# Performance work log

Measured on AMD Instinct MI355X. Metric: run time of the kernel, lower is better.

## Reference

```python
import jax, jax.numpy as jnp
import numpy as np

# Instant-NGP hash-encoding constants
PI = np.array([1, 2654435761, 805459861], dtype=np.uint32)
NUM_LEVELS = 16
MIN_RES = 16
MAX_RES = 512
T = 524288  # max entries per level (2**19)
D_EMBED = 2
N_POINTS = 2097152

# 8 binary corner offsets of a unit cube, shape [8, 3]
CORNERS = np.array([[(c >> d) & 1 for d in range(3)] for c in range(8)], dtype=np.int32)


def level_params():
    """Static per-level resolution, table size, offset, hashed flag."""
    b = (MAX_RES / MIN_RES) ** (1.0 / (NUM_LEVELS - 1))
    res = [int(np.floor(MIN_RES * b ** i)) for i in range(NUM_LEVELS)]
    sizes = [min((r + 1) ** 3, T) for r in res]
    offsets = np.concatenate([[0], np.cumsum(sizes)[:-1]]).astype(np.int32)
    hashed = [(r + 1) ** 3 > T for r in res]
    return res, sizes, offsets, hashed


RES, SIZES, OFFSETS, HASHED = level_params()
TOTAL_ENTRIES = int(np.sum(SIZES))


def setup_inputs() -> dict:
    key = jax.random.key(0)
    k1, k2 = jax.random.split(key)
    coords = jax.random.uniform(k1, (N_POINTS, 3), dtype=jnp.float32)
    embeddings = jax.random.normal(k2, (TOTAL_ENTRIES, D_EMBED), dtype=jnp.float32)
    return {"coords": coords, "embeddings": embeddings}


def _encode(coords, embeddings):
    corners = jnp.asarray(CORNERS)            # [8, 3] int32
    corner_mask = jnp.asarray(CORNERS, bool)  # [8, 3]
    pi = jnp.asarray(PI)                      # [3] uint32
    outs = []
    for lvl in range(NUM_LEVELS):
        res = RES[lvl]
        scaled = coords * res                                   # [N, 3]
        base = jnp.floor(scaled)
        frac = scaled - base                                    # [N, 3]
        # integer corner coords, clipped to valid grid range [0, res]
        c = jnp.clip(base.astype(jnp.int32)[:, None, :] + corners[None], 0, res)  # [N, 8, 3]
        if HASHED[lvl]:
            h = c.astype(jnp.uint32) * pi                        # wraparound mul, [N, 8, 3]
            idx = (h[..., 0] ^ h[..., 1] ^ h[..., 2]) % jnp.uint32(SIZES[lvl])
            idx = idx.astype(jnp.int32)                          # [N, 8]
        else:
            s = res + 1
            idx = c[..., 0] + c[..., 1] * s + c[..., 2] * (s * s)  # [N, 8]
        emb = embeddings[OFFSETS[lvl] + idx]                     # gather: [N, 8, d_embed]
        # trilinear weights: prod over dims of frac (corner=1) or 1-frac (corner=0)
        w = jnp.prod(jnp.where(corner_mask[None], frac[:, None, :], 1.0 - frac[:, None, :]), axis=-1)  # [N, 8]
        outs.append(jnp.einsum("nc,ncd->nd", w, emb))            # [N, d_embed]
    return jnp.concatenate(outs, axis=-1)                        # [N, L*d_embed]


def reference(coords, embeddings):
    return _encode(coords, embeddings)
```

## Files before the change

kernel.cpp:

```cpp
#include <hip/hip_runtime.h>
#include <math.h>

namespace {
constexpr int NPTS = 1 << 21;
constexpr int NLVL = 16;
constexpr unsigned TMASK = 0x7FFFFu;
constexpr unsigned PI1 = 2654435761u;
constexpr unsigned PI2 = 805459861u;
constexpr int BLK = 512;
constexpr int PTS_PER_BLK = 512;
constexpr int NBLK = NPTS / PTS_PER_BLK;
constexpr int NGRID = 7;
constexpr int NHASH = 9;
constexpr int BRES = 64;
constexpr int NBKT = BRES * BRES * BRES;

typedef float f2 __attribute__((ext_vector_type(2)));
typedef float f4 __attribute__((ext_vector_type(4)));
typedef unsigned u4 __attribute__((ext_vector_type(4)));

struct Params {
  float resf[NLVL];
  int off[NLVL];
  int cellOffB[NGRID];
  int hOffB[NHASH];
};

__device__ __forceinline__ int swz(int pt) { return (pt ^ (pt >> 3)) & 7; }

__device__ __forceinline__ unsigned bfrne(float x) {
  unsigned f = __float_as_uint(x);
  return (f + 0x7FFFu + ((f >> 16) & 1u)) >> 16;
}
__device__ __forceinline__ unsigned packbf(f2 e) {
  return bfrne(e.x) | (bfrne(e.y) << 16);
}
__device__ __forceinline__ float bflo(unsigned u) {
  return __uint_as_float(u << 16);
}
__device__ __forceinline__ float bfhi(unsigned u) {
  return __uint_as_float(u & 0xFFFF0000u);
}
__device__ __forceinline__ unsigned sel4(f4 v, int k) {
  float g = (k & 2) ? ((k & 1) ? v.w : v.z) : ((k & 1) ? v.y : v.x);
  return __float_as_uint(g);
}
__device__ __forceinline__ int bucket_of(float cx, float cy, float cz) {
  return (int)(cx * 64.f) + ((int)(cy * 64.f) << 6) + ((int)(cz * 64.f) << 12);
}
}

__global__ __launch_bounds__(256) void repack_all(const f2* __restrict__ emb,
                                                  char* __restrict__ ws,
                                                  Params p) {
  int y = (int)blockIdx.y;
  int t = (int)blockIdx.x * 256 + (int)threadIdx.x;
  if (y >= NGRID) {
    int h = y - NGRID;
    int off = p.off[7], hob = p.hOffB[0];
    if (h == 1) { off = p.off[8]; hob = p.hOffB[1]; }
    if (h == 2) { off = p.off[9]; hob = p.hOffB[2]; }
    if (h == 3) { off = p.off[10]; hob = p.hOffB[3]; }
    if (h == 4) { off = p.off[11]; hob = p.hOffB[4]; }
    if (h == 5) { off = p.off[12]; hob = p.hOffB[5]; }
    if (h == 6) { off = p.off[13]; hob = p.hOffB[6]; }
    if (h == 7) { off = p.off[14]; hob = p.hOffB[7]; }
    if (h == 8) { off = p.off[15]; hob = p.hOffB[8]; }
    ((unsigned*)(ws + (size_t)hob))[t] = packbf(emb[off + t]);
    return;
  }
  float rf = p.resf[0];
  int off = p.off[0], cob = p.cellOffB[0];
  if (y == 1) { rf = p.resf[1]; off = p.off[1]; cob = p.cellOffB[1]; }
  if (y == 2) { rf = p.resf[2]; off = p.off[2]; cob = p.cellOffB[2]; }
  if (y == 3) { rf = p.resf[3]; off = p.off[3]; cob = p.cellOffB[3]; }
  if (y == 4) { rf = p.resf[4]; off = p.off[4]; cob = p.cellOffB[4]; }
  if (y == 5) { rf = p.resf[5]; off = p.off[5]; cob = p.cellOffB[5]; }
  if (y == 6) { rf = p.resf[6]; off = p.off[6]; cob = p.cellOffB[6]; }
  int res = (int)rf;
  if (t >= res * res * res) return;
  int x = t % res, q = t / res, yy = q % res, z = q / res;
  int s = res + 1, s2 = s * s;
  const f2* base = emb + off + (x + yy * s + z * s2);
  u4 d0, d1;
  d0.x = packbf(base[0]);       d0.y = packbf(base[1]);
  d0.z = packbf(base[s]);       d0.w = packbf(base[s + 1]);
  d1.x = packbf(base[s2]);      d1.y = packbf(base[s2 + 1]);
  d1.z = packbf(base[s2 + s]);  d1.w = packbf(base[s2 + s + 1]);
  u4* dst = (u4*)(ws + (size_t)cob + (size_t)t * 32);
  dst[0] = d0; dst[1] = d1;
}

__global__ __launch_bounds__(256) void repack_grid(const f2* __restrict__ emb,
                                                   char* __restrict__ ws,
                                                   Params p) {
  int lvl = (int)blockIdx.y;
  float rf = p.resf[0];
  int off = p.off[0], cob = p.cellOffB[0];
  if (lvl == 1) { rf = p.resf[1]; off = p.off[1]; cob = p.cellOffB[1]; }
  if (lvl == 2) { rf = p.resf[2]; off = p.off[2]; cob = p.cellOffB[2]; }
  if (lvl == 3) { rf = p.resf[3]; off = p.off[3]; cob = p.cellOffB[3]; }
  if (lvl == 4) { rf = p.resf[4]; off = p.off[4]; cob = p.cellOffB[4]; }
  if (lvl == 5) { rf = p.resf[5]; off = p.off[5]; cob = p.cellOffB[5]; }
  if (lvl == 6) { rf = p.resf[6]; off = p.off[6]; cob = p.cellOffB[6]; }
  int res = (int)rf;
  int t = (int)blockIdx.x * 256 + (int)threadIdx.x;
  if (t >= res * res * res) return;
  int x = t % res, q = t / res, y = q % res, z = q / res;
  int s = res + 1, s2 = s * s;
  const f2* base = emb + off + (x + y * s + z * s2);
  u4 d0, d1;
  d0.x = packbf(base[0]);       d0.y = packbf(base[1]);
  d0.z = packbf(base[s]);       d0.w = packbf(base[s + 1]);
  d1.x = packbf(base[s2]);      d1.y = packbf(base[s2 + 1]);
  d1.z = packbf(base[s2 + s]);  d1.w = packbf(base[s2 + s + 1]);
  u4* dst = (u4*)(ws + (size_t)cob + (size_t)t * 32);
  dst[0] = d0; dst[1] = d1;
}

__global__ __launch_bounds__(256) void hist_k(const float* __restrict__ coords,
                                              unsigned* __restrict__ cnt) {
  int t = (int)blockIdx.x * 256 + (int)threadIdx.x;
  const f4* C = (const f4*)(coords + (size_t)t * 12);
  f4 a = C[0], b = C[1], c = C[2];
  atomicAdd(&cnt[bucket_of(a.x, a.y, a.z)], 1u);
  atomicAdd(&cnt[bucket_of(a.w, b.x, b.y)], 1u);
  atomicAdd(&cnt[bucket_of(b.z, b.w, c.x)], 1u);
  atomicAdd(&cnt[bucket_of(c.y, c.z, c.w)], 1u);
}

__global__ __launch_bounds__(256) void scan1_k(const unsigned* __restrict__ cnt,
                                               unsigned* __restrict__ scanA,
                                               unsigned* __restrict__ bsum) {
  __shared__ unsigned s[256];
  int t = (int)threadIdx.x, i = (int)blockIdx.x * 256 + t;
  unsigned v = cnt[i];
  s[t] = v;
  __syncthreads();
  for (int d = 1; d < 256; d <<= 1) {
    unsigned x = (t >= d) ? s[t - d] : 0u;
    __syncthreads();
    s[t] += x;
    __syncthreads();
  }
  scanA[i] = s[t] - v;
  if (t == 255) bsum[blockIdx.x] = s[255];
}

__global__ __launch_bounds__(1024) void scan2_k(unsigned* __restrict__ bsum) {
  __shared__ unsigned s[1024];
  int t = (int)threadIdx.x;
  unsigned v = bsum[t];
  s[t] = v;
  __syncthreads();
  for (int d = 1; d < 1024; d <<= 1) {
    unsigned x = (t >= d) ? s[t - d] : 0u;
    __syncthreads();
    s[t] += x;
    __syncthreads();
  }
  bsum[t] = s[t] - v;
}

__global__ __launch_bounds__(256) void scat_k(const float* __restrict__ coords,
                                              unsigned* __restrict__ scanA,
                                              const unsigned* __restrict__ bsum,
                                              f4* __restrict__ sorted) {
  int t = (int)blockIdx.x * 256 + (int)threadIdx.x;
  const f4* C = (const f4*)(coords + (size_t)t * 12);
  f4 a = C[0], b = C[1], c = C[2];
  unsigned n0 = (unsigned)(t * 4);
  int b0 = bucket_of(a.x, a.y, a.z);
  unsigned s0 = atomicAdd(&scanA[b0], 1u) + bsum[b0 >> 8];
  f4 v0; v0.x = a.x; v0.y = a.y; v0.z = a.z; v0.w = __uint_as_float(n0);
  sorted[s0] = v0;
  int b1 = bucket_of(a.w, b.x, b.y);
  unsigned s1 = atomicAdd(&scanA[b1], 1u) + bsum[b1 >> 8];
  f4 v1; v1.x = a.w; v1.y = b.x; v1.z = b.y; v1.w = __uint_as_float(n0 + 1u);
  sorted[s1] = v1;
  int b2 = bucket_of(b.z, b.w, c.x);
  unsigned s2 = atomicAdd(&scanA[b2], 1u) + bsum[b2 >> 8];
  f4 v2; v2.x = b.z; v2.y = b.w; v2.z = c.x; v2.w = __uint_as_float(n0 + 2u);
  sorted[s2] = v2;
  int b3 = bucket_of(c.y, c.z, c.w);
  unsigned s3 = atomicAdd(&scanA[b3], 1u) + bsum[b3 >> 8];
  f4 v3; v3.x = c.y; v3.y = c.z; v3.z = c.w; v3.w = __uint_as_float(n0 + 3u);
  sorted[s3] = v3;
}

struct GB {
  f4 l0, l1;
  float wx0, wx1, w00, w10, w01, w11;
};

template <int LVL>
__device__ __forceinline__ void gridb_issue(const Params& p,
                                            const char* __restrict__ ws,
                                            float cx, float cy, float cz,
                                            GB& s) {
  float rf = p.resf[LVL];
  int res = (int)rf;
  float sx = cx * rf, sy = cy * rf, sz = cz * rf;
  float bx = floorf(sx), by = floorf(sy), bz = floorf(sz);
  float fx = sx - bx, fy = sy - by, fz = sz - bz;
  int ix = (int)bx, iy = (int)by, iz = (int)bz;
  int cell = (iz * res + iy) * res + ix;
  const f4* src = (const f4*)(ws + (size_t)p.cellOffB[LVL] + (size_t)cell * 32);
  s.l0 = src[0]; s.l1 = src[1];
  float wy0 = 1.f - fy, wy1 = fy, wz0 = 1.f - fz, wz1 = fz;
  s.wx0 = 1.f - fx; s.wx1 = fx;
  s.w00 = wy0 * wz0; s.w10 = wy1 * wz0; s.w01 = wy0 * wz1; s.w11 = wy1 * wz1;
}

__device__ __forceinline__ f2 gridb_consume(const GB& s) {
  float a0 = 0.f, a1 = 0.f;
  unsigned u;
  u = __float_as_uint(s.l0.x); a0 = fmaf(s.wx0 * s.w00, bflo(u), a0); a1 = fmaf(s.wx0 * s.w00, bfhi(u), a1);
  u = __float_as_uint(s.l0.y); a0 = fmaf(s.wx1 * s.w00, bflo(u), a0); a1 = fmaf(s.wx1 * s.w00, bfhi(u), a1);
  u = __float_as_uint(s.l0.z); a0 = fmaf(s.wx0 * s.w10, bflo(u), a0); a1 = fmaf(s.wx0 * s.w10, bfhi(u), a1);
  u = __float_as_uint(s.l0.w); a0 = fmaf(s.wx1 * s.w10, bflo(u), a0); a1 = fmaf(s.wx1 * s.w10, bfhi(u), a1);
  u = __float_as_uint(s.l1.x); a0 = fmaf(s.wx0 * s.w01, bflo(u), a0); a1 = fmaf(s.wx0 * s.w01, bfhi(u), a1);
  u = __float_as_uint(s.l1.y); a0 = fmaf(s.wx1 * s.w01, bflo(u), a0); a1 = fmaf(s.wx1 * s.w01, bfhi(u), a1);
  u = __float_as_uint(s.l1.z); a0 = fmaf(s.wx0 * s.w11, bflo(u), a0); a1 = fmaf(s.wx0 * s.w11, bfhi(u), a1);
  u = __float_as_uint(s.l1.w); a0 = fmaf(s.wx1 * s.w11, bflo(u), a0); a1 = fmaf(s.wx1 * s.w11, bfhi(u), a1);
  f2 r; r.x = a0; r.y = a1;
  return r;
}

template <int LVL>
__device__ __forceinline__ f2 grid_direct(const Params& p,
                                          const f2* __restrict__ emb, float cx,
                                          float cy, float cz) {
  float rf = p.resf[LVL];
  int res = (int)rf;
  int s = res + 1, s2 = s * s;
  const f2* tab = emb + p.off[LVL];
  float sx = cx * rf, sy = cy * rf, sz = cz * rf;
  float bx = floorf(sx), by = floorf(sy), bz = floorf(sz);
  float fx = sx - bx, fy = sy - by, fz = sz - bz;
  int ix = (int)bx, iy = (int)by, iz = (int)bz;
  int bse = ix + iy * s + iz * s2;
  f2 e0 = tab[bse], e1 = tab[bse + 1];
  f2 e2 = tab[bse + s], e3 = tab[bse + s + 1];
  f2 e4 = tab[bse + s2], e5 = tab[bse + s2 + 1];
  f2 e6 = tab[bse + s2 + s], e7 = tab[bse + s2 + s + 1];
  float wx0 = 1.f - fx, wx1 = fx, wy0 = 1.f - fy, wy1 = fy;
  float wz0 = 1.f - fz, wz1 = fz;
  float w00 = wy0 * wz0, w10 = wy1 * wz0, w01 = wy0 * wz1, w11 = wy1 * wz1;
  float a0 = 0.f, a1 = 0.f;
  a0 = fmaf(wx0 * w00, e0.x, a0); a1 = fmaf(wx0 * w00, e0.y, a1);
  a0 = fmaf(wx1 * w00, e1.x, a0); a1 = fmaf(wx1 * w00, e1.y, a1);
  a0 = fmaf(wx0 * w10, e2.x, a0); a1 = fmaf(wx0 * w10, e2.y, a1);
  a0 = fmaf(wx1 * w10, e3.x, a0); a1 = fmaf(wx1 * w10, e3.y, a1);
  a0 = fmaf(wx0 * w01, e4.x, a0); a1 = fmaf(wx0 * w01, e4.y, a1);
  a0 = fmaf(wx1 * w01, e5.x, a0); a1 = fmaf(wx1 * w01, e5.y, a1);
  a0 = fmaf(wx0 * w11, e6.x, a0); a1 = fmaf(wx0 * w11, e6.y, a1);
  a0 = fmaf(wx1 * w11, e7.x, a0); a1 = fmaf(wx1 * w11, e7.y, a1);
  f2 r; r.x = a0; r.y = a1;
  return r;
}

struct HB {
  f4 cA0, cA1, cA2, cA3;
  unsigned uB0, uB1, uB2, uB3;
  float wA0, wB0, wA1, wB1, wA2, wB2, wA3, wB3;
  int kA0, kA1, kA2, kA3, kB0, kB1, kB2, kB3;
  bool sameChunk;
};

template <int LVL>
__device__ __forceinline__ void hashb_issue(const Params& p,
                                            const char* __restrict__ ws,
                                            float cx, float cy, float cz,
                                            HB& s) {
  float rf = p.resf[LVL];
  const f4* tab = (const f4*)(ws + (size_t)p.hOffB[LVL - 7]);
  const unsigned* t32 = (const unsigned*)tab;
  float sx = cx * rf, sy = cy * rf, sz = cz * rf;
  float bx = floorf(sx), by = floorf(sy), bz = floorf(sz);
  float fx = sx - bx, fy = sy - by, fz = sz - bz;
  unsigned ix = (unsigned)(int)bx, iy = (unsigned)(int)by,
           iz = (unsigned)(int)bz;
  unsigned jx = ix + 1u;
  unsigned ty0 = iy * PI1, ty1 = ty0 + PI1;
  unsigned tz0 = iz * PI2, tz1 = tz0 + PI2;
  unsigned e00 = ty0 ^ tz0, e10 = ty1 ^ tz0, e01 = ty0 ^ tz1, e11 = ty1 ^ tz1;
  float wx0 = 1.f - fx, wx1 = fx, wy0 = 1.f - fy, wy1 = fy;
  float wz0 = 1.f - fz, wz1 = fz;
  float w00 = wy0 * wz0, w10 = wy1 * wz0, w01 = wy0 * wz1, w11 = wy1 * wz1;
  unsigned iA0 = (ix ^ e00) & TMASK, iB0 = (jx ^ e00) & TMASK;
  unsigned iA1 = (ix ^ e10) & TMASK, iB1 = (jx ^ e10) & TMASK;
  unsigned iA2 = (ix ^ e01) & TMASK, iB2 = (jx ^ e01) & TMASK;
  unsigned iA3 = (ix ^ e11) & TMASK, iB3 = (jx ^ e11) & TMASK;
  s.sameChunk = (ix & 3u) != 3u;
  s.uB0 = 0u; s.uB1 = 0u; s.uB2 = 0u; s.uB3 = 0u;
  if (!s.sameChunk) {
    s.uB0 = t32[iB0]; s.uB1 = t32[iB1];
    s.uB2 = t32[iB2]; s.uB3 = t32[iB3];
  }
  s.cA0 = tab[iA0 >> 2]; s.cA1 = tab[iA1 >> 2];
  s.cA2 = tab[iA2 >> 2]; s.cA3 = tab[iA3 >> 2];
  s.kA0 = (int)(iA0 & 3u); s.kA1 = (int)(iA1 & 3u);
  s.kA2 = (int)(iA2 & 3u); s.kA3 = (int)(iA3 & 3u);
  s.kB0 = (int)(iB0 & 3u); s.kB1 = (int)(iB1 & 3u);
  s.kB2 = (int)(iB2 & 3u); s.kB3 = (int)(iB3 & 3u);
  s.wA0 = wx0 * w00; s.wB0 = wx1 * w00;
  s.wA1 = wx0 * w10; s.wB1 = wx1 * w10;
  s.wA2 = wx0 * w01; s.wB2 = wx1 * w01;
  s.wA3 = wx0 * w11; s.wB3 = wx1 * w11;
}

__device__ __forceinline__ void hbpair(f4 cA, unsigned uBl, int kA, int kB,
                                       bool same, float wA, float wB,
                                       float& a0, float& a1) {
  unsigned uA = sel4(cA, kA);
  unsigned uB = same ? sel4(cA, kB) : uBl;
  a0 = fmaf(wA, bflo(uA), a0); a1 = fmaf(wA, bfhi(uA), a1);
  a0 = fmaf(wB, bflo(uB), a0); a1 = fmaf(wB, bfhi(uB), a1);
}

__device__ __forceinline__ f2 hashb_consume(const HB& s) {
  float a0 = 0.f, a1 = 0.f;
  hbpair(s.cA0, s.uB0, s.kA0, s.kB0, s.sameChunk, s.wA0, s.wB0, a0, a1);
  hbpair(s.cA1, s.uB1, s.kA1, s.kB1, s.sameChunk, s.wA1, s.wB1, a0, a1);
  hbpair(s.cA2, s.uB2, s.kA2, s.kB2, s.sameChunk, s.wA2, s.wB2, a0, a1);
  hbpair(s.cA3, s.uB3, s.kA3, s.kB3, s.sameChunk, s.wA3, s.wB3, a0, a1);
  f2 r; r.x = a0; r.y = a1;
  return r;
}

struct HS {
  f4 lo0, hi0, lo1, hi1, lo2, hi2, lo3, hi3;
  float wA0, wB0, wA1, wB1, wA2, wB2, wA3, wB3;
  int oA0, oB0, oA1, oB1, oA2, oB2, oA3, oB3;
};

template <int LVL>
__device__ __forceinline__ void hash_issue(const Params& p,
                                           const f2* __restrict__ emb,
                                           float cx, float cy, float cz,
                                           HS& s) {
  float rf = p.resf[LVL];
  const f2* tab = emb + p.off[LVL];
  float sx = cx * rf, sy = cy * rf, sz = cz * rf;
  float bx = floorf(sx), by = floorf(sy), bz = floorf(sz);
  float fx = sx - bx, fy = sy - by, fz = sz - bz;
  unsigned ix = (unsigned)(int)bx, iy = (unsigned)(int)by,
           iz = (unsigned)(int)bz;
  unsigned jx = ix + 1u;
  unsigned ty0 = iy * PI1, ty1 = ty0 + PI1;
  unsigned tz0 = iz * PI2, tz1 = tz0 + PI2;
  unsigned e00 = ty0 ^ tz0, e10 = ty1 ^ tz0, e01 = ty0 ^ tz1, e11 = ty1 ^ tz1;
  float wx0 = 1.f - fx, wx1 = fx, wy0 = 1.f - fy, wy1 = fy;
  float wz0 = 1.f - fz, wz1 = fz;
  float w00 = wy0 * wz0, w10 = wy1 * wz0, w01 = wy0 * wz1, w11 = wy1 * wz1;
  unsigned iA, iB;
  iA = (ix ^ e00) & TMASK; iB = (jx ^ e00) & TMASK;
  s.oA0 = (int)(iA & 1u); s.oB0 = (int)(iB & 1u);
  s.lo0 = *(const f4*)(tab + (iA & ~1u)); s.hi0 = *(const f4*)(tab + (iB & ~1u));
  s.wA0 = wx0 * w00; s.wB0 = wx1 * w00;
  iA = (ix ^ e10) & TMASK; iB = (jx ^ e10) & TMASK;
  s.oA1 = (int)(iA & 1u); s.oB1 = (int)(iB & 1u);
  s.lo1 = *(const f4*)(tab + (iA & ~1u)); s.hi1 = *(const f4*)(tab + (iB & ~1u));
  s.wA1 = wx0 * w10; s.wB1 = wx1 * w10;
  iA = (ix ^ e01) & TMASK; iB = (jx ^ e01) & TMASK;
  s.oA2 = (int)(iA & 1u); s.oB2 = (int)(iB & 1u);
  s.lo2 = *(const f4*)(tab + (iA & ~1u)); s.hi2 = *(const f4*)(tab + (iB & ~1u));
  s.wA2 = wx0 * w01; s.wB2 = wx1 * w01;
  iA = (ix ^ e11) & TMASK; iB = (jx ^ e11) & TMASK;
  s.oA3 = (int)(iA & 1u); s.oB3 = (int)(iB & 1u);
  s.lo3 = *(const f4*)(tab + (iA & ~1u)); s.hi3 = *(const f4*)(tab + (iB & ~1u));
  s.wA3 = wx0 * w11; s.wB3 = wx1 * w11;
}

__device__ __forceinline__ void hpair2(f4 lo, f4 hi, int oA, int oB, float wA,
                                       float wB, float& a0, float& a1) {
  float eAx = oA ? lo.z : lo.x, eAy = oA ? lo.w : lo.y;
  float eBx = oB ? hi.z : hi.x, eBy = oB ? hi.w : hi.y;
  a0 = fmaf(wA, eAx, a0); a1 = fmaf(wA, eAy, a1);
  a0 = fmaf(wB, eBx, a0); a1 = fmaf(wB, eBy, a1);
}

__device__ __forceinline__ f2 hash_consume(const HS& s) {
  float a0 = 0.f, a1 = 0.f;
  hpair2(s.lo0, s.hi0, s.oA0, s.oB0, s.wA0, s.wB0, a0, a1);
  hpair2(s.lo1, s.hi1, s.oA1, s.oB1, s.wA1, s.wB1, a0, a1);
  hpair2(s.lo2, s.hi2, s.oA2, s.oB2, s.wA2, s.wB2, a0, a1);
  hpair2(s.lo3, s.hi3, s.oA3, s.oB3, s.wA3, s.wB3, a0, a1);
  f2 r; r.x = a0; r.y = a1;
  return r;
}

template <int LVL, int MODE>
__device__ __forceinline__ void do_phase(const Params& p,
                                         const f2* __restrict__ emb,
                                         const char* __restrict__ ws, float cx,
                                         float cy, float cz, int pt,
                                         unsigned* lds) {
  f2 r;
  if constexpr (LVL < NGRID) {
    if constexpr (MODE < 2) {
      GB s;
      gridb_issue<LVL>(p, ws, cx, cy, cz, s);
      r = gridb_consume(s);
    } else {
      r = grid_direct<LVL>(p, emb, cx, cy, cz);
    }
  } else {
    if constexpr (MODE == 0) {
      HB s;
      hashb_issue<LVL>(p, ws, cx, cy, cz, s);
      r = hashb_consume(s);
    } else {
      HS s;
      hash_issue<LVL>(p, emb, cx, cy, cz, s);
      r = hash_consume(s);
    }
  }
  lds[pt * 8 + ((LVL & 7) ^ swz(pt))] = packbf(r);
}

template <bool SORTED>
__device__ __forceinline__ void readout(float* __restrict__ out,
                                        const unsigned* lds,
                                        const unsigned* oiLds, int n0, int h,
                                        int tid) {
#pragma unroll
  for (int j = 0; j < 4; ++j) {
    int f = tid + BLK * j;
    int pt = f >> 2, k = f & 3;
    int s = swz(pt);
    unsigned u0 = lds[pt * 8 + ((2 * k) ^ s)];
    unsigned u1 = lds[pt * 8 + ((2 * k + 1) ^ s)];
    f4 o4; o4.x = bflo(u0); o4.y = bfhi(u0); o4.z = bflo(u1); o4.w = bfhi(u1);
    size_t base = SORTED ? (size_t)oiLds[pt] * 32 : (size_t)(n0 + pt) * 32;
    __builtin_nontemporal_store(o4, (f4*)(out + base + h * 16 + k * 4));
  }
}

template <int MODE, bool SORTED>
__global__ __launch_bounds__(BLK, 4) void henc(const float* __restrict__ coords,
                                               const f2* __restrict__ emb,
                                               float* __restrict__ out,
                                               const char* __restrict__ ws,
                                               const f4* __restrict__ sorted,
                                               Params p) {
  __shared__ unsigned lds[PTS_PER_BLK * 8];
  __shared__ unsigned oiLds[PTS_PER_BLK];
  const int tid = (int)threadIdx.x;
  const int n0 = (int)blockIdx.x * PTS_PER_BLK;
  const int pt = tid;

  float cx, cy, cz;
  if constexpr (SORTED) {
    f4 s0 = sorted[n0 + pt];
    cx = s0.x; cy = s0.y; cz = s0.z;
    oiLds[pt] = __float_as_uint(s0.w);
  } else {
    cx = coords[3 * (n0 + pt) + 0];
    cy = coords[3 * (n0 + pt) + 1];
    cz = coords[3 * (n0 + pt) + 2];
  }

  do_phase<0, MODE>(p, emb, ws, cx, cy, cz, pt, lds);
  do_phase<1, MODE>(p, emb, ws, cx, cy, cz, pt, lds);
  do_phase<2, MODE>(p, emb, ws, cx, cy, cz, pt, lds);
  do_phase<3, MODE>(p, emb, ws, cx, cy, cz, pt, lds);
  do_phase<4, MODE>(p, emb, ws, cx, cy, cz, pt, lds);
  do_phase<5, MODE>(p, emb, ws, cx, cy, cz, pt, lds);
  do_phase<6, MODE>(p, emb, ws, cx, cy, cz, pt, lds);
  do_phase<7, MODE>(p, emb, ws, cx, cy, cz, pt, lds);
  __syncthreads();
  readout<SORTED>(out, lds, oiLds, n0, 0, tid);
  __syncthreads();

  do_phase<8, MODE>(p, emb, ws, cx, cy, cz, pt, lds);
  do_phase<9, MODE>(p, emb, ws, cx, cy, cz, pt, lds);
  do_phase<10, MODE>(p, emb, ws, cx, cy, cz, pt, lds);
  do_phase<11, MODE>(p, emb, ws, cx, cy, cz, pt, lds);
  do_phase<12, MODE>(p, emb, ws, cx, cy, cz, pt, lds);
  do_phase<13, MODE>(p, emb, ws, cx, cy, cz, pt, lds);
  do_phase<14, MODE>(p, emb, ws, cx, cy, cz, pt, lds);
  do_phase<15, MODE>(p, emb, ws, cx, cy, cz, pt, lds);
  __syncthreads();
  readout<SORTED>(out, lds, oiLds, n0, 1, tid);
}

extern "C" void kernel_launch(void* const* d_in, const int* in_sizes, int n_in,
                              void* d_out, int out_size, void* d_ws,
                              size_t ws_size, hipStream_t stream) {
  const float* coords = (const float*)d_in[0];
  const f2* emb = (const f2*)d_in[1];
  float* out = (float*)d_out;
  char* ws = (char*)d_ws;

  Params p;
  double b = pow(32.0, 1.0 / 15.0);
  long long cum = 0, cellCum = 0;
  int resMax = 64;
  for (int i = 0; i < NLVL; ++i) {
    int r = (int)floor(16.0 * pow(b, (double)i));
    p.resf[i] = (float)r;
    p.off[i] = (int)cum;
    long long e3 = (long long)(r + 1) * (r + 1) * (r + 1);
    cum += e3 > 524288 ? 524288 : e3;
    if (i < NGRID) {
      p.cellOffB[i] = (int)(cellCum * 32);
      cellCum += (long long)r * r * r;
      if (i == NGRID - 1) resMax = r;
    }
  }
  long long gridB = ((cellCum * 32 + 63) / 64) * 64;
  for (int h = 0; h < NHASH; ++h)
    p.hOffB[h] = (int)(gridB + (long long)h * (524288 * 4));
  size_t needB = (size_t)gridB;
  size_t needA = (size_t)(gridB + 9LL * 524288 * 4);

  size_t cntOff = (needA + 255) & ~(size_t)255;
  size_t scanOff = cntOff + (size_t)NBKT * 4;
  size_t bsumOff = scanOff + (size_t)NBKT * 4;
  size_t sortedOff = (bsumOff + 4096 + 255) & ~(size_t)255;
  size_t needS = sortedOff + (size_t)NPTS * 16;

  int mode = ws_size >= needA ? 0 : (ws_size >= needB ? 1 : 2);
  bool doSort = ws_size >= needS;

  if (mode == 0) {
    repack_all<<<dim3(524288 / 256, NLVL), dim3(256), 0, stream>>>(emb, ws, p);
    if (doSort) {
      unsigned* cnt = (unsigned*)(ws + cntOff);
      unsigned* scanA = (unsigned*)(ws + scanOff);
      unsigned* bsum = (unsigned*)(ws + bsumOff);
      f4* sorted = (f4*)(ws + sortedOff);
      hipMemsetAsync(cnt, 0, (size_t)NBKT * 4, stream);
      hist_k<<<dim3(NPTS / 4 / 256), dim3(256), 0, stream>>>(coords, cnt);
      scan1_k<<<dim3(NBKT / 256), dim3(256), 0, stream>>>(cnt, scanA, bsum);
      scan2_k<<<dim3(1), dim3(1024), 0, stream>>>(bsum);
      scat_k<<<dim3(NPTS / 4 / 256), dim3(256), 0, stream>>>(coords, scanA,
                                                             bsum, sorted);
      henc<0, true><<<dim3(NBLK), dim3(BLK), 0, stream>>>(coords, emb, out, ws,
                                                          sorted, p);
    } else {
      henc<0, false><<<dim3(NBLK), dim3(BLK), 0, stream>>>(coords, emb, out,
                                                           ws, nullptr, p);
    }
  } else if (mode == 1) {
    int bx = (resMax * resMax * resMax + 255) / 256;
    repack_grid<<<dim3(bx, NGRID), dim3(256), 0, stream>>>(emb, ws, p);
    henc<1, false><<<dim3(NBLK), dim3(BLK), 0, stream>>>(coords, emb, out, ws,
                                                         nullptr, p);
  } else {
    henc<2, false><<<dim3(NBLK), dim3(BLK), 0, stream>>>(coords, emb, out, ws,
                                                         nullptr, p);
  }
}
```

Measured before the change: 467.7 us.

## Fuse point bucket sort into a single cooperative kernel with grid syncs

```diff
diff --git a/kernel.cpp b/kernel.cpp
--- a/kernel.cpp
+++ b/kernel.cpp
@@ -1,5 +1,8 @@
 #include <hip/hip_runtime.h>
+#include <hip/hip_cooperative_groups.h>
 #include <math.h>
+
+namespace cg = cooperative_groups;
 
 namespace {
 constexpr int NPTS = 1 << 21;
@@ -14,6 +17,8 @@
 constexpr int NHASH = 9;
 constexpr int BRES = 64;
 constexpr int NBKT = BRES * BRES * BRES;
+constexpr int SORT_BLKS = 2048;
+constexpr int SORT_THR = 256;
 
 typedef float f2 __attribute__((ext_vector_type(2)));
 typedef float f4 __attribute__((ext_vector_type(4)));
@@ -116,6 +121,81 @@
   d1.z = packbf(base[s2 + s]);  d1.w = packbf(base[s2 + s + 1]);
   u4* dst = (u4*)(ws + (size_t)cob + (size_t)t * 32);
   dst[0] = d0; dst[1] = d1;
+}
+
+__global__ __launch_bounds__(SORT_THR) void sort_coop(
+    const float* __restrict__ coords, unsigned* __restrict__ cnt,
+    unsigned* __restrict__ excl, unsigned* __restrict__ bsum,
+    f4* __restrict__ sorted) {
+  cg::grid_group grid = cg::this_grid();
+  __shared__ unsigned s[256];
+  const int tid = (int)blockIdx.x * SORT_THR + (int)threadIdx.x;
+
+  if (tid < NBKT) cnt[tid] = 0u;
+  grid.sync();
+
+  const f4* C = (const f4*)(coords + (size_t)tid * 12);
+  f4 a = C[0], b = C[1], c = C[2];
+  int b0 = bucket_of(a.x, a.y, a.z);
+  int b1 = bucket_of(a.w, b.x, b.y);
+  int b2 = bucket_of(b.z, b.w, c.x);
+  int b3 = bucket_of(c.y, c.z, c.w);
+  unsigned r0 = atomicAdd(&cnt[b0], 1u);
+  unsigned r1 = atomicAdd(&cnt[b1], 1u);
+  unsigned r2 = atomicAdd(&cnt[b2], 1u);
+  unsigned r3 = atomicAdd(&cnt[b3], 1u);
+  grid.sync();
+
+  if (blockIdx.x < NBKT / 256) {
+    int t = (int)threadIdx.x, i = (int)blockIdx.x * 256 + t;
+    unsigned v = cnt[i];
+    s[t] = v;
+    __syncthreads();
+    for (int d = 1; d < 256; d <<= 1) {
+      unsigned x = (t >= d) ? s[t - d] : 0u;
+      __syncthreads();
+      s[t] += x;
+      __syncthreads();
+    }
+    excl[i] = s[t] - v;
+    if (t == 255) bsum[blockIdx.x] = s[255];
+  }
+  grid.sync();
+
+  if (blockIdx.x == 0) {
+    int t = (int)threadIdx.x;
+    unsigned v0 = bsum[4 * t], v1 = bsum[4 * t + 1];
+    unsigned v2 = bsum[4 * t + 2], v3 = bsum[4 * t + 3];
+    unsigned tot = v0 + v1 + v2 + v3;
+    s[t] = tot;
+    __syncthreads();
+    for (int d = 1; d < 256; d <<= 1) {
+      unsigned x = (t >= d) ? s[t - d] : 0u;
+      __syncthreads();
+      s[t] += x;
+      __syncthreads();
+    }
+    unsigned base = s[t] - tot;
+    bsum[4 * t] = base;
+    bsum[4 * t + 1] = base + v0;
+    bsum[4 * t + 2] = base + v0 + v1;
+    bsum[4 * t + 3] = base + v0 + v1 + v2;
+  }
+  grid.sync();
+
+  unsigned n0 = (unsigned)(tid * 4);
+  unsigned s0 = excl[b0] + bsum[b0 >> 8] + r0;
+  f4 v0; v0.x = a.x; v0.y = a.y; v0.z = a.z; v0.w = __uint_as_float(n0);
+  sorted[s0] = v0;
+  unsigned s1 = excl[b1] + bsum[b1 >> 8] + r1;
+  f4 v1; v1.x = a.w; v1.y = b.x; v1.z = b.y; v1.w = __uint_as_float(n0 + 1u);
+  sorted[s1] = v1;
+  unsigned s2 = excl[b2] + bsum[b2 >> 8] + r2;
+  f4 v2; v2.x = b.z; v2.y = b.w; v2.z = c.x; v2.w = __uint_as_float(n0 + 2u);
+  sorted[s2] = v2;
+  unsigned s3 = excl[b3] + bsum[b3 >> 8] + r3;
+  f4 v3; v3.x = c.y; v3.y = c.z; v3.z = c.w; v3.w = __uint_as_float(n0 + 3u);
+  sorted[s3] = v3;
 }
 
 __global__ __launch_bounds__(256) void hist_k(const float* __restrict__ coords,
@@ -517,8 +597,8 @@
   size_t needA = (size_t)(gridB + 9LL * 524288 * 4);
 
   size_t cntOff = (needA + 255) & ~(size_t)255;
-  size_t scanOff = cntOff + (size_t)NBKT * 4;
-  size_t bsumOff = scanOff + (size_t)NBKT * 4;
+  size_t exclOff = cntOff + (size_t)NBKT * 4;
+  size_t bsumOff = exclOff + (size_t)NBKT * 4;
   size_t sortedOff = (bsumOff + 4096 + 255) & ~(size_t)255;
   size_t needS = sortedOff + (size_t)NPTS * 16;
 
@@ -529,15 +609,30 @@
     repack_all<<<dim3(524288 / 256, NLVL), dim3(256), 0, stream>>>(emb, ws, p);
     if (doSort) {
       unsigned* cnt = (unsigned*)(ws + cntOff);
-      unsigned* scanA = (unsigned*)(ws + scanOff);
+      unsigned* excl = (unsigned*)(ws + exclOff);
       unsigned* bsum = (unsigned*)(ws + bsumOff);
       f4* sorted = (f4*)(ws + sortedOff);
-      hipMemsetAsync(cnt, 0, (size_t)NBKT * 4, stream);
-      hist_k<<<dim3(NPTS / 4 / 256), dim3(256), 0, stream>>>(coords, cnt);
-      scan1_k<<<dim3(NBKT / 256), dim3(256), 0, stream>>>(cnt, scanA, bsum);
-      scan2_k<<<dim3(1), dim3(1024), 0, stream>>>(bsum);
-      scat_k<<<dim3(NPTS / 4 / 256), dim3(256), 0, stream>>>(coords, scanA,
-                                                             bsum, sorted);
+
+      bool coopOk = false;
+      int nb = 0;
+      if (hipOccupancyMaxActiveBlocksPerMultiprocessor(
+              &nb, (const void*)sort_coop, SORT_THR, 0) == hipSuccess &&
+          nb >= (SORT_BLKS + 255) / 256) {
+        void* args[] = {(void*)&coords, (void*)&cnt, (void*)&excl,
+                        (void*)&bsum, (void*)&sorted};
+        if (hipLaunchCooperativeKernel((const void*)sort_coop,
+                                       dim3(SORT_BLKS), dim3(SORT_THR), args,
+                                       0, stream) == hipSuccess)
+          coopOk = true;
+      }
+      if (!coopOk) {
+        hipMemsetAsync(cnt, 0, (size_t)NBKT * 4, stream);
+        hist_k<<<dim3(NPTS / 4 / 256), dim3(256), 0, stream>>>(coords, cnt);
+        scan1_k<<<dim3(NBKT / 256), dim3(256), 0, stream>>>(cnt, excl, bsum);
+        scan2_k<<<dim3(1), dim3(1024), 0, stream>>>(bsum);
+        scat_k<<<dim3(NPTS / 4 / 256), dim3(256), 0, stream>>>(coords, excl,
+                                                               bsum, sorted);
+      }
       henc<0, true><<<dim3(NBLK), dim3(BLK), 0, stream>>>(coords, emb, out, ws,
                                                           sorted, p);
     } else {
```

Measured after the change: 467.9 us. Within noise of the previous version (+0.0%).
